# Performance work log

Hardware: AMD Instinct MI355X
Metric: run time of the kernel (lower is better)

The kernel has to match this reference:

```python
import jax, jax.numpy as jnp
import numpy as np

ALPHA = 0.95   # membrane leak factor exp(-dt/tau_mem)
RHO   = 0.98   # threshold-adaptation decay
BETA  = 1.8    # adaptive threshold gain (ALIF)
TH0   = 1.0    # base threshold
SCALE = 10.0   # SuperSpike surrogate slope

@jax.custom_vjp
def spike(v):
    # Heaviside spike with SuperSpike surrogate gradient (as in cantata's SurrGradSpike)
    return (v >= 0.0).astype(v.dtype)

def _spike_fwd(v):
    return spike(v), v

def _spike_bwd(v, g):
    return (g / (SCALE * jnp.abs(v) + 1.0) ** 2,)

spike.defvjp(_spike_fwd, _spike_bwd)

def _onehot_delays(k, n, d):
    # each presynaptic source is routed through exactly one delay bin
    idx = jax.random.randint(k, (n,), 0, d)
    return (jnp.arange(d)[:, None] == idx[None, :]).astype(jnp.float32)  # [d, n]

def setup_inputs() -> dict:
    B, N, D, NE, DE = 32, 4096, 8, 2048, 4
    key = jax.random.key(0)
    ks = jax.random.split(key, 8)
    V = jax.random.normal(ks[0], (B, N), jnp.float32)
    a = jax.random.uniform(ks[1], (B, N), jnp.float32)
    Xd = (jax.random.uniform(ks[2], (D, B, N)) < 0.05).astype(jnp.float32)      # internal delay ring buffer
    Xext = (jax.random.uniform(ks[3], (DE, B, NE)) < 0.05).astype(jnp.float32)  # delayed external spikes
    W_int = jax.random.normal(ks[4], (N, N), jnp.float32) * 0.02
    W_ext = jax.random.normal(ks[5], (NE, N), jnp.float32) * 0.02
    dmap_int = _onehot_delays(ks[6], N, D)
    dmap_ext = _onehot_delays(ks[7], NE, DE)
    return dict(V=V, a=a, Xd=Xd, Xext=Xext, W_int=W_int, W_ext=W_ext,
                dmap_int=dmap_int, dmap_ext=dmap_ext)

def reference(V, a, Xd, Xext, W_int, W_ext, dmap_int, dmap_ext):
    # 1) ALIF spike generation from membrane + adaptive threshold
    th = TH0 + BETA * a
    X = spike(V - th)                                     # [B,N]
    a_new = RHO * a + X
    # 2) push new spikes into the delay ring buffer (delay 0 = current step)
    Xd_new = jnp.concatenate([X[None], Xd[:-1]], axis=0)  # [D,B,N]
    # 3) delay-mapped synaptic current: gather each presyn source from its delay bin,
    #    then dense delta-synapse accumulation (internal + cross-area)
    x_int = jnp.einsum('dbi,di->bi', Xd_new, dmap_int)    # [B,N]
    x_ext = jnp.einsum('dbi,di->bi', Xext, dmap_ext)      # [B,NE]
    current = x_int @ W_int + x_ext @ W_ext               # [B,N]
    # 4) membrane update: leak, reset on spike, integrate current
    V_new = ALPHA * V * (1.0 - X) + current
    return jnp.stack([X, V_new, a_new])                   # [3,B,N]
```

## Files before the change

### kernel.cpp

```cpp
#include <hip/hip_runtime.h>


#define B_   32
#define N_   4096
#define D_   8
#define NE_  2048
#define DE_  4
#define BN_  (B_ * N_)
#define BNE_ (B_ * NE_)
#define NCH_ 8
#define CI_  512
#define CE_  256

__global__ __launch_bounds__(256) void snn_spike_compact(
    const float* __restrict__ V, const float* __restrict__ a,
    const float* __restrict__ Xd, const float* __restrict__ Xext,
    const float* __restrict__ dmap_int, const float* __restrict__ dmap_ext,
    float* __restrict__ out,
    int* __restrict__ cnt_int, int* __restrict__ cnt_ext,
    unsigned short* __restrict__ list_int, unsigned short* __restrict__ list_ext)
{
#pragma clang fp contract(off)
    __shared__ unsigned short s_i[CI_];
    __shared__ unsigned short s_e[CE_];
    __shared__ int lc_i, lc_e;
    int tid = threadIdx.x;
    if (tid == 0) { lc_i = 0; lc_e = 0; }
    __syncthreads();

    int b = blockIdx.y;
    int c = blockIdx.x;

    #pragma unroll
    for (int r = 0; r < 2; ++r) {
        int i = c * CI_ + r * 256 + tid;
        int t = b * N_ + i;
        float av = a[t];
        float vv = V[t];
        float th = 1.0f + 1.8f * av;
        float x = (vv - th >= 0.0f) ? 1.0f : 0.0f;
        out[t] = x;
        out[2 * BN_ + t] = 0.98f * av + x;
        int di = 0;
        #pragma unroll
        for (int d = 1; d < D_; ++d)
            if (dmap_int[d * N_ + i] != 0.0f) di = d;
        float xi = (di == 0) ? x : Xd[(di - 1) * BN_ + t];
        if (xi != 0.0f) {
            int p = atomicAdd(&lc_i, 1);
            s_i[p] = (unsigned short)i;
        }
    }
    {
        int j = c * CE_ + tid;
        int u = b * NE_ + j;
        int de = 0;
        #pragma unroll
        for (int d = 1; d < DE_; ++d)
            if (dmap_ext[d * NE_ + j] != 0.0f) de = d;
        float xe = Xext[de * BNE_ + u];
        if (xe != 0.0f) {
            int p = atomicAdd(&lc_e, 1);
            s_e[p] = (unsigned short)j;
        }
    }
    __syncthreads();
    if (tid == 0) {
        cnt_int[b * NCH_ + c] = lc_i;
        cnt_ext[b * NCH_ + c] = lc_e;
    }
    for (int k = tid; k < lc_i; k += 256) list_int[b * N_  + c * CI_ + k] = s_i[k];
    for (int k = tid; k < lc_e; k += 256) list_ext[b * NE_ + c * CE_ + k] = s_e[k];
}

__device__ __forceinline__ float4 ld4(const float* p) { return *(const float4*)p; }
__device__ __forceinline__ void add4(float4& a, const float4 w) {
    a.x += w.x; a.y += w.y; a.z += w.z; a.w += w.w;
}

__device__ __forceinline__ void accum_rows(const float* __restrict__ W,
                                           const unsigned short* sl, int n, int j,
                                           float4& acc)
{
    if (n <= 0) return;
    int nf = n & ~7;
    if (nf >= 8) {
        uint4 g = *(const uint4*)(sl);
        float4 p0 = ld4(W + (size_t)(g.x & 0xffff) * N_ + j);
        float4 p1 = ld4(W + (size_t)(g.x >> 16)    * N_ + j);
        float4 p2 = ld4(W + (size_t)(g.y & 0xffff) * N_ + j);
        float4 p3 = ld4(W + (size_t)(g.y >> 16)    * N_ + j);
        float4 p4 = ld4(W + (size_t)(g.z & 0xffff) * N_ + j);
        float4 p5 = ld4(W + (size_t)(g.z >> 16)    * N_ + j);
        float4 p6 = ld4(W + (size_t)(g.w & 0xffff) * N_ + j);
        float4 p7 = ld4(W + (size_t)(g.w >> 16)    * N_ + j);
        for (int k = 8; k < nf; k += 8) {
            uint4 g2 = *(const uint4*)(sl + k);
            float4 q0 = ld4(W + (size_t)(g2.x & 0xffff) * N_ + j);
            float4 q1 = ld4(W + (size_t)(g2.x >> 16)    * N_ + j);
            float4 q2 = ld4(W + (size_t)(g2.y & 0xffff) * N_ + j);
            float4 q3 = ld4(W + (size_t)(g2.y >> 16)    * N_ + j);
            float4 q4 = ld4(W + (size_t)(g2.z & 0xffff) * N_ + j);
            float4 q5 = ld4(W + (size_t)(g2.z >> 16)    * N_ + j);
            float4 q6 = ld4(W + (size_t)(g2.w & 0xffff) * N_ + j);
            float4 q7 = ld4(W + (size_t)(g2.w >> 16)    * N_ + j);
            add4(acc, p0); add4(acc, p1); add4(acc, p2); add4(acc, p3);
            add4(acc, p4); add4(acc, p5); add4(acc, p6); add4(acc, p7);
            p0 = q0; p1 = q1; p2 = q2; p3 = q3;
            p4 = q4; p5 = q5; p6 = q6; p7 = q7;
        }
        add4(acc, p0); add4(acc, p1); add4(acc, p2); add4(acc, p3);
        add4(acc, p4); add4(acc, p5); add4(acc, p6); add4(acc, p7);
    }
    for (int k = nf; k < n; ++k) {
        float4 w = ld4(W + (size_t)sl[k] * N_ + j);
        add4(acc, w);
    }
}

__global__ __launch_bounds__(512, 4) void snn_current(
    const float* __restrict__ W_int, const float* __restrict__ W_ext,
    const float* __restrict__ V, float* __restrict__ out,
    const int* __restrict__ cnt_int, const int* __restrict__ cnt_ext,
    const unsigned short* __restrict__ list_int,
    const unsigned short* __restrict__ list_ext)
{
    __shared__ __align__(16) unsigned short s_int[N_];
    __shared__ __align__(16) unsigned short s_ext[NE_];
    __shared__ float4 s_part[8][64];
    int tid = threadIdx.x;
    int b = blockIdx.y;

    int ci[NCH_], oi[NCH_], ce[NCH_], oe[NCH_];
    int ni = 0, ne = 0;
    #pragma unroll
    for (int c = 0; c < NCH_; ++c) {
        ci[c] = cnt_int[b * NCH_ + c]; oi[c] = ni; ni += ci[c];
        ce[c] = cnt_ext[b * NCH_ + c]; oe[c] = ne; ne += ce[c];
    }
    #pragma unroll
    for (int c = 0; c < NCH_; ++c) {
        for (int k = tid; k < ci[c]; k += 512) s_int[oi[c] + k] = list_int[b * N_  + c * CI_ + k];
        for (int k = tid; k < ce[c]; k += 512) s_ext[oe[c] + k] = list_ext[b * NE_ + c * CE_ + k];
    }
    __syncthreads();

    int w = tid >> 6, lane = tid & 63;
    int j = blockIdx.x * 256 + lane * 4;
    float4 acc = make_float4(0.f, 0.f, 0.f, 0.f);

    int qi = ((ni + 63) >> 6) << 3;
    int si = w * qi;
    accum_rows(W_int, s_int + si, min(ni, si + qi) - si, j, acc);
    int qe = ((ne + 63) >> 6) << 3;
    int se = w * qe;
    accum_rows(W_ext, s_ext + se, min(ne, se + qe) - se, j, acc);

    s_part[w][lane] = acc;
    __syncthreads();

    if (tid < 256) {
        const float* spf = (const float*)s_part;
        float cur = 0.0f;
        #pragma unroll
        for (int ww = 0; ww < 8; ++ww) cur += spf[ww * 256 + tid];
        int t = b * N_ + blockIdx.x * 256 + tid;
        float v = V[t];
        float x = out[t];
        out[BN_ + t] = 0.95f * v * (1.0f - x) + cur;
    }
}

extern "C" void kernel_launch(void* const* d_in, const int* in_sizes, int n_in,
                              void* d_out, int out_size, void* d_ws, size_t ws_size,
                              hipStream_t stream)
{
    const float* V        = (const float*)d_in[0];
    const float* a        = (const float*)d_in[1];
    const float* Xd       = (const float*)d_in[2];
    const float* Xext     = (const float*)d_in[3];
    const float* W_int    = (const float*)d_in[4];
    const float* W_ext    = (const float*)d_in[5];
    const float* dmap_int = (const float*)d_in[6];
    const float* dmap_ext = (const float*)d_in[7];
    float* out = (float*)d_out;

    int* cnt_int = (int*)d_ws;
    int* cnt_ext = (int*)((char*)d_ws + 1024);
    unsigned short* list_int = (unsigned short*)((char*)d_ws + 2048);
    unsigned short* list_ext = (unsigned short*)((char*)d_ws + 2048 + (size_t)BN_ * 2);

    dim3 g1(NCH_, B_);
    snn_spike_compact<<<g1, 256, 0, stream>>>(
        V, a, Xd, Xext, dmap_int, dmap_ext, out, cnt_int, cnt_ext, list_int, list_ext);

    dim3 g2(16, B_);
    snn_current<<<g2, 512, 0, stream>>>(
        W_int, W_ext, V, out, cnt_int, cnt_ext, list_int, list_ext);
}
```

Baseline: 144.3 us.

## Narrow current kernel tiles to 128 columns with float2 loads and 4 waves

Reworks the sparse-row gather kernel so each block covers 128 output columns with 256 threads. Each lane now loads float2 instead of float4, and the spike list is split across 4 waves instead of 8. The grid doubles to 32x32 blocks to add parallelism. In exchange, each lane's gather is narrower (8-byte loads, 512 bytes per wave per row), each block recopies the spike lists into shared memory, and each wave now walks a twice-longer slice of the spike list.

After: 148.5 us. 3.0% more time.

```diff
diff --git a/kernel.cpp b/kernel.cpp
--- a/kernel.cpp
+++ b/kernel.cpp
@@ -73,52 +73,52 @@
     for (int k = tid; k < lc_e; k += 256) list_ext[b * NE_ + c * CE_ + k] = s_e[k];
 }
 
-__device__ __forceinline__ float4 ld4(const float* p) { return *(const float4*)p; }
-__device__ __forceinline__ void add4(float4& a, const float4 w) {
-    a.x += w.x; a.y += w.y; a.z += w.z; a.w += w.w;
-}
-
-__device__ __forceinline__ void accum_rows(const float* __restrict__ W,
-                                           const unsigned short* sl, int n, int j,
-                                           float4& acc)
+__device__ __forceinline__ float2 ld2(const float* p) { return *(const float2*)p; }
+__device__ __forceinline__ void add2(float2& a, const float2 w) {
+    a.x += w.x; a.y += w.y;
+}
+
+__device__ __forceinline__ void accum_rows2(const float* __restrict__ W,
+                                            const unsigned short* sl, int n, int j,
+                                            float2& acc)
 {
     if (n <= 0) return;
     int nf = n & ~7;
     if (nf >= 8) {
         uint4 g = *(const uint4*)(sl);
-        float4 p0 = ld4(W + (size_t)(g.x & 0xffff) * N_ + j);
-        float4 p1 = ld4(W + (size_t)(g.x >> 16)    * N_ + j);
-        float4 p2 = ld4(W + (size_t)(g.y & 0xffff) * N_ + j);
-        float4 p3 = ld4(W + (size_t)(g.y >> 16)    * N_ + j);
-        float4 p4 = ld4(W + (size_t)(g.z & 0xffff) * N_ + j);
-        float4 p5 = ld4(W + (size_t)(g.z >> 16)    * N_ + j);
-        float4 p6 = ld4(W + (size_t)(g.w & 0xffff) * N_ + j);
-        float4 p7 = ld4(W + (size_t)(g.w >> 16)    * N_ + j);
+        float2 p0 = ld2(W + (size_t)(g.x & 0xffff) * N_ + j);
+        float2 p1 = ld2(W + (size_t)(g.x >> 16)    * N_ + j);
+        float2 p2 = ld2(W + (size_t)(g.y & 0xffff) * N_ + j);
+        float2 p3 = ld2(W + (size_t)(g.y >> 16)    * N_ + j);
+        float2 p4 = ld2(W + (size_t)(g.z & 0xffff) * N_ + j);
+        float2 p5 = ld2(W + (size_t)(g.z >> 16)    * N_ + j);
+        float2 p6 = ld2(W + (size_t)(g.w & 0xffff) * N_ + j);
+        float2 p7 = ld2(W + (size_t)(g.w >> 16)    * N_ + j);
         for (int k = 8; k < nf; k += 8) {
             uint4 g2 = *(const uint4*)(sl + k);
-            float4 q0 = ld4(W + (size_t)(g2.x & 0xffff) * N_ + j);
-            float4 q1 = ld4(W + (size_t)(g2.x >> 16)    * N_ + j);
-            float4 q2 = ld4(W + (size_t)(g2.y & 0xffff) * N_ + j);
-            float4 q3 = ld4(W + (size_t)(g2.y >> 16)    * N_ + j);
-            float4 q4 = ld4(W + (size_t)(g2.z & 0xffff) * N_ + j);
-            float4 q5 = ld4(W + (size_t)(g2.z >> 16)    * N_ + j);
-            float4 q6 = ld4(W + (size_t)(g2.w & 0xffff) * N_ + j);
-            float4 q7 = ld4(W + (size_t)(g2.w >> 16)    * N_ + j);
-            add4(acc, p0); add4(acc, p1); add4(acc, p2); add4(acc, p3);
-            add4(acc, p4); add4(acc, p5); add4(acc, p6); add4(acc, p7);
+            float2 q0 = ld2(W + (size_t)(g2.x & 0xffff) * N_ + j);
+            float2 q1 = ld2(W + (size_t)(g2.x >> 16)    * N_ + j);
+            float2 q2 = ld2(W + (size_t)(g2.y & 0xffff) * N_ + j);
+            float2 q3 = ld2(W + (size_t)(g2.y >> 16)    * N_ + j);
+            float2 q4 = ld2(W + (size_t)(g2.z & 0xffff) * N_ + j);
+            float2 q5 = ld2(W + (size_t)(g2.z >> 16)    * N_ + j);
+            float2 q6 = ld2(W + (size_t)(g2.w & 0xffff) * N_ + j);
+            float2 q7 = ld2(W + (size_t)(g2.w >> 16)    * N_ + j);
+            add2(acc, p0); add2(acc, p1); add2(acc, p2); add2(acc, p3);
+            add2(acc, p4); add2(acc, p5); add2(acc, p6); add2(acc, p7);
             p0 = q0; p1 = q1; p2 = q2; p3 = q3;
             p4 = q4; p5 = q5; p6 = q6; p7 = q7;
         }
-        add4(acc, p0); add4(acc, p1); add4(acc, p2); add4(acc, p3);
-        add4(acc, p4); add4(acc, p5); add4(acc, p6); add4(acc, p7);
+        add2(acc, p0); add2(acc, p1); add2(acc, p2); add2(acc, p3);
+        add2(acc, p4); add2(acc, p5); add2(acc, p6); add2(acc, p7);
     }
     for (int k = nf; k < n; ++k) {
-        float4 w = ld4(W + (size_t)sl[k] * N_ + j);
-        add4(acc, w);
-    }
-}
-
-__global__ __launch_bounds__(512, 4) void snn_current(
+        float2 w = ld2(W + (size_t)sl[k] * N_ + j);
+        add2(acc, w);
+    }
+}
+
+__global__ __launch_bounds__(256, 4) void snn_current(
     const float* __restrict__ W_int, const float* __restrict__ W_ext,
     const float* __restrict__ V, float* __restrict__ out,
     const int* __restrict__ cnt_int, const int* __restrict__ cnt_ext,
@@ -127,7 +127,7 @@
 {
     __shared__ __align__(16) unsigned short s_int[N_];
     __shared__ __align__(16) unsigned short s_ext[NE_];
-    __shared__ float4 s_part[8][64];
+    __shared__ float2 s_part[4][64];
     int tid = threadIdx.x;
     int b = blockIdx.y;
 
@@ -140,31 +140,31 @@
     }
     #pragma unroll
     for (int c = 0; c < NCH_; ++c) {
-        for (int k = tid; k < ci[c]; k += 512) s_int[oi[c] + k] = list_int[b * N_  + c * CI_ + k];
-        for (int k = tid; k < ce[c]; k += 512) s_ext[oe[c] + k] = list_ext[b * NE_ + c * CE_ + k];
+        for (int k = tid; k < ci[c]; k += 256) s_int[oi[c] + k] = list_int[b * N_  + c * CI_ + k];
+        for (int k = tid; k < ce[c]; k += 256) s_ext[oe[c] + k] = list_ext[b * NE_ + c * CE_ + k];
     }
     __syncthreads();
 
     int w = tid >> 6, lane = tid & 63;
-    int j = blockIdx.x * 256 + lane * 4;
-    float4 acc = make_float4(0.f, 0.f, 0.f, 0.f);
-
-    int qi = ((ni + 63) >> 6) << 3;
+    int j = blockIdx.x * 128 + lane * 2;
+    float2 acc = make_float2(0.f, 0.f);
+
+    int qi = ((ni + 31) >> 5) << 3;
     int si = w * qi;
-    accum_rows(W_int, s_int + si, min(ni, si + qi) - si, j, acc);
-    int qe = ((ne + 63) >> 6) << 3;
+    accum_rows2(W_int, s_int + si, min(ni, si + qi) - si, j, acc);
+    int qe = ((ne + 31) >> 5) << 3;
     int se = w * qe;
-    accum_rows(W_ext, s_ext + se, min(ne, se + qe) - se, j, acc);
+    accum_rows2(W_ext, s_ext + se, min(ne, se + qe) - se, j, acc);
 
     s_part[w][lane] = acc;
     __syncthreads();
 
-    if (tid < 256) {
+    if (tid < 128) {
         const float* spf = (const float*)s_part;
         float cur = 0.0f;
         #pragma unroll
-        for (int ww = 0; ww < 8; ++ww) cur += spf[ww * 256 + tid];
-        int t = b * N_ + blockIdx.x * 256 + tid;
+        for (int ww = 0; ww < 4; ++ww) cur += spf[ww * 128 + tid];
+        int t = b * N_ + blockIdx.x * 128 + tid;
         float v = V[t];
         float x = out[t];
         out[BN_ + t] = 0.95f * v * (1.0f - x) + cur;
@@ -194,7 +194,7 @@
     snn_spike_compact<<<g1, 256, 0, stream>>>(
         V, a, Xd, Xext, dmap_int, dmap_ext, out, cnt_int, cnt_ext, list_int, list_ext);
 
-    dim3 g2(16, B_);
-    snn_current<<<g2, 512, 0, stream>>>(
+    dim3 g2(32, B_);
+    snn_current<<<g2, 256, 0, stream>>>(
         W_int, W_ext, V, out, cnt_int, cnt_ext, list_int, list_ext);
 }
```
